# Kernel optimization log

Measured on AMD Instinct MI355X. Metric: run time of the kernel, lower is better.

The kernel has to match this reference:

```python
import jax, jax.numpy as jnp
import numpy as np

B, H, W, C = 16, 56, 56, 384
HEADS, WIN, SHIFT = 12, 7, 3
HD = C // HEADS
HIDDEN = 4 * C
NWH, NWW = H // WIN, W // WIN
NW = NWH * NWW
WA = WIN * WIN  # 49 tokens per window


def _rel_pos_index():
    coords = np.stack(np.meshgrid(np.arange(WIN), np.arange(WIN), indexing='ij')).reshape(2, -1)
    rel = coords[:, :, None] - coords[:, None, :]          # [2, WA, WA]
    rel = rel.transpose(1, 2, 0)
    rel[:, :, 0] += WIN - 1
    rel[:, :, 1] += WIN - 1
    rel[:, :, 0] *= 2 * WIN - 1
    return rel.sum(-1)                                      # [WA, WA]


def _attn_mask():
    img = np.zeros((H, W))
    cnt = 0
    for hs in (slice(0, -WIN), slice(-WIN, -SHIFT), slice(-SHIFT, None)):
        for ws in (slice(0, -WIN), slice(-WIN, -SHIFT), slice(-SHIFT, None)):
            img[hs, ws] = cnt
            cnt += 1
    mw = img.reshape(NWH, WIN, NWW, WIN).transpose(0, 2, 1, 3).reshape(NW, WA)
    diff = mw[:, None, :] - mw[:, :, None]
    return np.where(diff != 0, -100.0, 0.0).astype(np.float32)  # [NW, WA, WA]


REL_IDX = jnp.asarray(_rel_pos_index())
MASK = jnp.asarray(_attn_mask())


def _ln(x, g, b):
    m = x.mean(-1, keepdims=True)
    v = ((x - m) ** 2).mean(-1, keepdims=True)
    return (x - m) / jnp.sqrt(v + 1e-5) * g + b


def setup_inputs() -> dict:
    key = jax.random.key(0)
    ks = jax.random.split(key, 6)
    s = 0.02
    return {
        'x': jax.random.normal(ks[0], (B, H, W, C), jnp.float32),
        'norm1_g': jnp.ones((C,), jnp.float32),
        'norm1_b': jnp.zeros((C,), jnp.float32),
        'qkv_w': jax.random.normal(ks[1], (C, 3 * C), jnp.float32) * s,
        'qkv_b': jnp.zeros((3 * C,), jnp.float32),
        'rel_bias': jax.random.normal(ks[2], ((2 * WIN - 1) ** 2, HEADS), jnp.float32) * s,
        'proj_w': jax.random.normal(ks[3], (C, C), jnp.float32) * s,
        'proj_b': jnp.zeros((C,), jnp.float32),
        'norm2_g': jnp.ones((C,), jnp.float32),
        'norm2_b': jnp.zeros((C,), jnp.float32),
        'fc1_w': jax.random.normal(ks[4], (C, HIDDEN), jnp.float32) * s,
        'fc1_b': jnp.zeros((HIDDEN,), jnp.float32),
        'fc2_w': jax.random.normal(ks[5], (HIDDEN, C), jnp.float32) * s,
        'fc2_b': jnp.zeros((C,), jnp.float32),
    }


def reference(x, norm1_g, norm1_b, qkv_w, qkv_b, rel_bias, proj_w, proj_b,
              norm2_g, norm2_b, fc1_w, fc1_b, fc2_w, fc2_b):
    # ---- shifted-window attention branch ----
    xs = _ln(x, norm1_g, norm1_b)
    xs = jnp.roll(xs, (-SHIFT, -SHIFT), axis=(1, 2))
    # window partition: [B,H,W,C] -> [B*NW, WA, C]
    xw = xs.reshape(B, NWH, WIN, NWW, WIN, C).transpose(0, 1, 3, 2, 4, 5).reshape(B * NW, WA, C)
    qkv = (xw @ qkv_w + qkv_b).reshape(B * NW, WA, 3, HEADS, HD)
    q = qkv[:, :, 0].transpose(0, 2, 1, 3)  # [bw, heads, WA, HD]
    k = qkv[:, :, 1].transpose(0, 2, 1, 3)
    v = qkv[:, :, 2].transpose(0, 2, 1, 3)
    attn = jnp.einsum('bhqd,bhkd->bhqk', q, k) * (HD ** -0.5)
    bias = rel_bias[REL_IDX].transpose(2, 0, 1)  # [heads, WA, WA]
    attn = attn + bias[None]
    attn = attn.reshape(B, NW, HEADS, WA, WA) + MASK[None, :, None]
    attn = jax.nn.softmax(attn, axis=-1).reshape(B * NW, HEADS, WA, WA)
    out = jnp.einsum('bhqk,bhkd->bhqd', attn, v).transpose(0, 2, 1, 3).reshape(B * NW, WA, C)
    out = out @ proj_w + proj_b
    # window reverse + unshift
    out = out.reshape(B, NWH, NWW, WIN, WIN, C).transpose(0, 1, 3, 2, 4, 5).reshape(B, H, W, C)
    out = jnp.roll(out, (SHIFT, SHIFT), axis=(1, 2))
    x = x + out
    # ---- MLP branch ----
    xf = x.reshape(B, H * W, C)
    h = _ln(xf, norm2_g, norm2_b)
    h = jax.nn.gelu(h @ fc1_w + fc1_b, approximate=False)
    xf = xf + (h @ fc2_w + fc2_b)
    return xf.reshape(B, H, W, C)
```

## Files before the change

### kernel.cpp

```cpp
#include <hip/hip_runtime.h>
#include <hip/hip_bf16.h>
#include <math.h>

#define NBATCH 16
#define NW 64
#define WA 49
#define NTOK (NBATCH*NW*WA)
#define CCH 384
#define HIDDEN 1536

typedef __attribute__((ext_vector_type(8))) short short8;
typedef __attribute__((ext_vector_type(4))) float floatx4;

static __device__ __forceinline__ short f2bf(float f){
  unsigned u = __float_as_uint(f);
  unsigned r = (u + 0x7fff + ((u>>16)&1)) >> 16;
  return (short)r;
}
static __device__ __forceinline__ float bf2f(short s){
  return __uint_as_float(((unsigned)(unsigned short)s)<<16);
}

static __device__ __forceinline__ void gload16(const void* g, void* l){
  __builtin_amdgcn_global_load_lds(
      (const __attribute__((address_space(1))) void*)g,
      (__attribute__((address_space(3))) void*)l, 16, 0, 0);
}

static __device__ __forceinline__ short8 ds_read_b128s(unsigned addr){
  short8 r;
  asm volatile("ds_read_b128 %0, %1" : "=v"(r) : "v"(addr));
  return r;
}
static __device__ __forceinline__ long ds_read_b64s(unsigned addr){
  long r;
  asm volatile("ds_read_b64 %0, %1" : "=v"(r) : "v"(addr));
  return r;
}

template<int N> __device__ __forceinline__ void waitvm();
template<> __device__ __forceinline__ void waitvm<0>(){ asm volatile("s_waitcnt vmcnt(0)" ::: "memory"); }
template<> __device__ __forceinline__ void waitvm<5>(){ asm volatile("s_waitcnt vmcnt(5)" ::: "memory"); }

static __device__ __forceinline__ int tok2pix(int t){
  int b = t / (NW*WA);
  int rem = t % (NW*WA);
  int w = rem / WA, a = rem % WA;
  int hs = (w>>3)*7 + a/7;
  int ws = (w&7)*7 + a%7;
  int hp = hs + 3; if (hp >= 56) hp -= 56;
  int wp = ws + 3; if (wp >= 56) wp -= 56;
  return (b*56 + hp)*56 + wp;
}

__global__ void wtconv(const float* __restrict__ W, short* __restrict__ Wt, int K, int N){
  int i = blockIdx.x*256 + threadIdx.x;
  if (i >= K*N) return;
  int k = i / N, n = i % N;
  Wt[(size_t)n*K + k] = f2bf(W[i]);
}

__global__ void wtconv8(const float* __restrict__ W, unsigned char* __restrict__ Wt, int K, int N){
  int i = blockIdx.x*256 + threadIdx.x;
  if (i >= K*N) return;
  int k = i / N, n = i % N;
  unsigned pk = (unsigned)__builtin_amdgcn_cvt_pk_fp8_f32(W[i], W[i], 0, false);
  Wt[(size_t)n*K + k] = (unsigned char)(pk & 0xff);
}

__global__ void rbt(const float* __restrict__ rb, float* __restrict__ rbT){
  int i = blockIdx.x*256 + threadIdx.x;
  if (i >= 169*12) return;
  int t = i / 12, h = i % 12;
  rbT[h*169 + t] = rb[i];
}

template<int MAP>
__global__ __launch_bounds__(256) void ln_fp8(const float* __restrict__ x,
    const float* __restrict__ g, const float* __restrict__ bta, unsigned char* __restrict__ out){
  int wid = threadIdx.x>>6, lane = threadIdx.x&63;
  int t = blockIdx.x*4 + wid;
  const float* row = x + (size_t)(MAP ? tok2pix(t) : t)*CCH;
  float v[8]; float s=0.f, ss=0.f;
  if (lane < 48){
    float4 p0 = *(const float4*)&row[lane*8];
    float4 p1 = *(const float4*)&row[lane*8+4];
    v[0]=p0.x;v[1]=p0.y;v[2]=p0.z;v[3]=p0.w;
    v[4]=p1.x;v[5]=p1.y;v[6]=p1.z;v[7]=p1.w;
    #pragma unroll
    for (int i=0;i<8;i++){ s+=v[i]; ss+=v[i]*v[i]; }
  }
  #pragma unroll
  for (int off=32; off; off>>=1){ s += __shfl_xor(s,off); ss += __shfl_xor(ss,off); }
  float mean = s*(1.f/384.f);
  float var  = ss*(1.f/384.f) - mean*mean;
  float inv  = rsqrtf(var + 1e-5f);
  if (lane < 48){
    float4 g0 = *(const float4*)&g[lane*8],  g1 = *(const float4*)&g[lane*8+4];
    float4 b0 = *(const float4*)&bta[lane*8],b1 = *(const float4*)&bta[lane*8+4];
    float o[8];
    o[0]=(v[0]-mean)*inv*g0.x+b0.x; o[1]=(v[1]-mean)*inv*g0.y+b0.y;
    o[2]=(v[2]-mean)*inv*g0.z+b0.z; o[3]=(v[3]-mean)*inv*g0.w+b0.w;
    o[4]=(v[4]-mean)*inv*g1.x+b1.x; o[5]=(v[5]-mean)*inv*g1.y+b1.y;
    o[6]=(v[6]-mean)*inv*g1.z+b1.z; o[7]=(v[7]-mean)*inv*g1.w+b1.w;
    unsigned w0 = (unsigned)__builtin_amdgcn_cvt_pk_fp8_f32(o[0], o[1], 0, false);
    w0 = (unsigned)__builtin_amdgcn_cvt_pk_fp8_f32(o[2], o[3], (int)w0, true);
    unsigned w1 = (unsigned)__builtin_amdgcn_cvt_pk_fp8_f32(o[4], o[5], 0, false);
    w1 = (unsigned)__builtin_amdgcn_cvt_pk_fp8_f32(o[6], o[7], (int)w1, true);
    uint2 pk; pk.x = w0; pk.y = w1;
    *(uint2*)&out[(size_t)t*CCH + lane*8] = pk;
  }
}

template<int EPI, int KK>
__global__ __launch_bounds__(512) void gemm8(const short* __restrict__ A,
    const short* __restrict__ Bt, const float* __restrict__ bias,
    const float* __restrict__ res, void* __restrict__ outp,
    int N, int gx)
{
  __shared__ short As[2][256][64];
  __shared__ short Bs[2][64][64];
  const int tid = threadIdx.x, lane = tid & 63, wid = tid >> 6;
  const int fr = lane & 15, fg = lane >> 4;
  const int wm = wid >> 1, wn = wid & 1;

  const int nwg = gridDim.x;
  const int q = nwg >> 3, r = nwg & 7;
  const int xcd = blockIdx.x & 7, pos = blockIdx.x >> 3;
  const int wgid = (xcd < r ? xcd*(q+1) : r*(q+1) + (xcd-r)*q) + pos;
  const int m0 = (wgid / gx) * 256, n0 = (wgid % gx) * 64;

  floatx4 acc[4][2];
  #pragma unroll
  for (int m=0;m<4;m++)
    #pragma unroll
    for (int n=0;n<2;n++) acc[m][n] = (floatx4){0.f,0.f,0.f,0.f};

  const int srow = tid >> 3;
  const int scol = ((tid & 7) ^ (srow & 7)) * 8;
  const short* gA = A  + (size_t)(m0 + srow) * KK + scol;
  const short* gB = Bt + (size_t)(n0 + srow) * KK + scol;
  constexpr int a64 = 64 * KK;
  short* aB = &As[0][wid*8][0];
  short* bB = &Bs[0][wid*8][0];
  constexpr int nt = KK >> 6;

  const unsigned aLds = (unsigned)(uintptr_t)&As[0][0][0];
  const unsigned bLds = (unsigned)(uintptr_t)&Bs[0][0][0];
  const unsigned rowOffA = (unsigned)((wm*64 + fr)*128);
  const unsigned rowOffB = (unsigned)((wn*32 + fr)*128);
  const unsigned pc0 = (unsigned)(((fg  ) ^ (fr&7))*16);
  const unsigned pc1 = (unsigned)(((4+fg) ^ (fr&7))*16);

#define STAGE(tt, bb) do{                                             \
    const int k0_ = (tt) << 6;                                        \
    short* a_ = aB + (bb)*256*64;                                     \
    short* b_ = bB + (bb)*64*64;                                      \
    gload16(gA + k0_,          a_);                                   \
    gload16(gA + k0_ +   a64,  a_ +  64*64);                          \
    gload16(gA + k0_ + 2*a64,  a_ + 128*64);                          \
    gload16(gA + k0_ + 3*a64,  a_ + 192*64);                          \
    gload16(gB + k0_,          b_);                                   \
  }while(0)

  STAGE(0, 0);
  #pragma unroll
  for (int t = 0; t < nt; ++t){
    const int buf = t & 1;
    if (t + 1 < nt){
      STAGE(t+1, buf^1);
      waitvm<5>();
    } else {
      waitvm<0>();
    }
    __builtin_amdgcn_s_barrier();
    const unsigned aoff = aLds + (unsigned)buf*32768u + rowOffA;
    const unsigned boff = bLds + (unsigned)buf*8192u  + rowOffB;
    #pragma unroll
    for (int kk=0; kk<2; ++kk){
      const unsigned pc = kk ? pc1 : pc0;
      short8 af[4], bq[2];
      #pragma unroll
      for (int m=0;m<4;m++) af[m] = ds_read_b128s(aoff + (unsigned)(m*2048) + pc);
      #pragma unroll
      for (int n=0;n<2;n++) bq[n] = ds_read_b128s(boff + (unsigned)(n*2048) + pc);
      asm volatile("s_waitcnt lgkmcnt(0)" ::: "memory");
      __builtin_amdgcn_sched_barrier(0);
      __builtin_amdgcn_s_setprio(1);
      #pragma unroll
      for (int m=0;m<4;m++)
        #pragma unroll
        for (int n=0;n<2;n++)
          acc[m][n] = __builtin_amdgcn_mfma_f32_16x16x32_bf16(af[m], bq[n], acc[m][n], 0,0,0);
      __builtin_amdgcn_s_setprio(0);
    }
    __builtin_amdgcn_s_barrier();
  }
#undef STAGE

  __syncthreads();
  float* Cl = (float*)&As[0][0][0];
  #pragma unroll
  for (int n=0;n<2;n++){
    int col = wn*32 + n*16 + fr;
    float bv = bias[n0 + col];
    #pragma unroll
    for (int m=0;m<4;m++){
      #pragma unroll
      for (int i=0;i<4;i++){
        int row = wm*64 + m*16 + fg*4 + i;
        Cl[row*64 + col] = acc[m][n][i] + bv;
      }
    }
  }
  __syncthreads();
  const int rr = tid >> 4, slot = tid & 15;
  #pragma unroll
  for (int it=0; it<8; ++it){
    int row = it*32 + rr;
    float4 v = *(const float4*)&Cl[row*64 + slot*4];
    int p = tok2pix(m0+row);
    size_t idx = (size_t)p*CCH + n0 + slot*4;
    float4 rv = *(const float4*)&res[idx];
    v.x += rv.x; v.y += rv.y; v.z += rv.z; v.w += rv.w;
    *(float4*)&((float*)outp)[idx] = v;
  }
}

template<int EPI, int KK>
__global__ __launch_bounds__(512) void gemmF8(const unsigned char* __restrict__ A8,
    const unsigned char* __restrict__ B8, const float* __restrict__ bias,
    const float* __restrict__ res, void* __restrict__ outp,
    int N, int gx)
{
  __shared__ unsigned char As8[2][256][128];
  __shared__ unsigned char Bs8[2][64][128];
  const int tid = threadIdx.x, lane = tid & 63, wid = tid >> 6;
  const int fr = lane & 15, fg = lane >> 4;
  const int wm = wid >> 1, wn = wid & 1;

  const int nwg = gridDim.x;
  const int q = nwg >> 3, r = nwg & 7;
  const int xcd = blockIdx.x & 7, pos = blockIdx.x >> 3;
  const int wgid = (xcd < r ? xcd*(q+1) : r*(q+1) + (xcd-r)*q) + pos;
  const int m0 = (wgid / gx) * 256, n0 = (wgid % gx) * 64;

  floatx4 acc[4][2];
  #pragma unroll
  for (int m=0;m<4;m++)
    #pragma unroll
    for (int n=0;n<2;n++) acc[m][n] = (floatx4){0.f,0.f,0.f,0.f};

  const int srow = tid >> 3;
  const int scolb = ((tid & 7) ^ (srow & 7)) * 16;
  const unsigned char* gA = A8 + (size_t)(m0 + srow) * KK + scolb;
  const unsigned char* gB = B8 + (size_t)(n0 + srow) * KK + scolb;
  constexpr int a64 = 64 * KK;
  unsigned char* aB = &As8[0][wid*8][0];
  unsigned char* bB = &Bs8[0][wid*8][0];
  constexpr int nt = KK >> 7;

  const unsigned aLds = (unsigned)(uintptr_t)&As8[0][0][0];
  const unsigned bLds = (unsigned)(uintptr_t)&Bs8[0][0][0];
  const unsigned rowOffA = (unsigned)((wm*64 + fr)*128);
  const unsigned rowOffB = (unsigned)((wn*32 + fr)*128);
  unsigned pcc[4];
  #pragma unroll
  for (int kk=0;kk<4;kk++)
    pcc[kk] = (unsigned)((((kk*2 + (fg>>1)) ^ (fr&7))*16) + (fg&1)*8);

#define STAGE8(tt, bb) do{                                            \
    const int k0_ = (tt) << 7;                                        \
    unsigned char* a_ = aB + (bb)*256*128;                            \
    unsigned char* b_ = bB + (bb)*64*128;                             \
    gload16(gA + k0_,          a_);                                   \
    gload16(gA + k0_ +   a64,  a_ +  8192);                           \
    gload16(gA + k0_ + 2*a64,  a_ + 16384);                           \
    gload16(gA + k0_ + 3*a64,  a_ + 24576);                           \
    gload16(gB + k0_,          b_);                                   \
  }while(0)

  STAGE8(0, 0);
  #pragma unroll
  for (int t = 0; t < nt; ++t){
    const int buf = t & 1;
    if (t + 1 < nt){
      STAGE8(t+1, buf^1);
      waitvm<5>();
    } else {
      waitvm<0>();
    }
    __builtin_amdgcn_s_barrier();
    const unsigned aoff = aLds + (unsigned)buf*32768u + rowOffA;
    const unsigned boff = bLds + (unsigned)buf*8192u  + rowOffB;
    #pragma unroll
    for (int kk=0; kk<4; ++kk){
      const unsigned pc = pcc[kk];
      long af[4], bq[2];
      #pragma unroll
      for (int m=0;m<4;m++) af[m] = ds_read_b64s(aoff + (unsigned)(m*2048) + pc);
      #pragma unroll
      for (int n=0;n<2;n++) bq[n] = ds_read_b64s(boff + (unsigned)(n*2048) + pc);
      asm volatile("s_waitcnt lgkmcnt(0)" ::: "memory");
      __builtin_amdgcn_sched_barrier(0);
      __builtin_amdgcn_s_setprio(1);
      #pragma unroll
      for (int m=0;m<4;m++)
        #pragma unroll
        for (int n=0;n<2;n++)
          acc[m][n] = __builtin_amdgcn_mfma_f32_16x16x32_fp8_fp8(af[m], bq[n], acc[m][n], 0,0,0);
      __builtin_amdgcn_s_setprio(0);
    }
    __builtin_amdgcn_s_barrier();
  }
#undef STAGE8

  __syncthreads();
  if (EPI==0){
    short* Cl = (short*)&As8[0][0][0];
    #pragma unroll
    for (int n=0;n<2;n++){
      int col = wn*32 + n*16 + fr;
      float bv = bias[n0 + col];
      #pragma unroll
      for (int m=0;m<4;m++){
        #pragma unroll
        for (int i=0;i<4;i++){
          int row = wm*64 + m*16 + fg*4 + i;
          Cl[row*64 + col] = f2bf(acc[m][n][i] + bv);
        }
      }
    }
    __syncthreads();
    const int rr = tid >> 3, slot = tid & 7;
    #pragma unroll
    for (int it=0; it<4; ++it){
      int row = it*64 + rr;
      short8 v = *(const short8*)&Cl[row*64 + slot*8];
      *(short8*)&((short*)outp)[(size_t)(m0+row)*N + n0 + slot*8] = v;
    }
  } else if (EPI==2){
    unsigned char* Cl = (unsigned char*)&As8[0][0][0];
    #pragma unroll
    for (int n=0;n<2;n++){
      int col = wn*32 + n*16 + fr;
      float bv = bias[n0 + col];
      #pragma unroll
      for (int m=0;m<4;m++){
        #pragma unroll
        for (int i=0;i<4;i++){
          int row = wm*64 + m*16 + fg*4 + i;
          float v = acc[m][n][i] + bv;
          float e2 = __expf(-1.702f*v);
          float gg = v * __builtin_amdgcn_rcpf(1.f + e2);
          unsigned pk = (unsigned)__builtin_amdgcn_cvt_pk_fp8_f32(gg, gg, 0, false);
          Cl[row*64 + col] = (unsigned char)(pk & 0xff);
        }
      }
    }
    __syncthreads();
    const int rr = tid >> 2, slot = tid & 3;
    #pragma unroll
    for (int it=0; it<2; ++it){
      int row = it*128 + rr;
      short8 v = *(const short8*)&Cl[row*64 + slot*16];
      *(short8*)&((unsigned char*)outp)[(size_t)(m0+row)*N + n0 + slot*16] = v;
    }
  } else {
    float* Cl = (float*)&As8[0][0][0];
    #pragma unroll
    for (int n=0;n<2;n++){
      int col = wn*32 + n*16 + fr;
      float bv = bias[n0 + col];
      #pragma unroll
      for (int m=0;m<4;m++){
        #pragma unroll
        for (int i=0;i<4;i++){
          int row = wm*64 + m*16 + fg*4 + i;
          Cl[row*64 + col] = acc[m][n][i] + bv;
        }
      }
    }
    __syncthreads();
    const int rr = tid >> 4, slot = tid & 15;
    #pragma unroll
    for (int it=0; it<8; ++it){
      int row = it*32 + rr;
      float4 v = *(const float4*)&Cl[row*64 + slot*4];
      size_t idx = (size_t)(m0+row)*CCH + n0 + slot*4;
      float4 rv = *(const float4*)&res[idx];
      v.x += rv.x; v.y += rv.y; v.z += rv.z; v.w += rv.w;
      *(float4*)&((float*)outp)[idx] = v;
    }
  }
}

__global__ __launch_bounds__(256) void attn_mfma(const short* __restrict__ qkv,
    const float* __restrict__ rbT, short* __restrict__ attnout)
{
  __shared__ short Pl[4][64][68];
  __shared__ short Vt[4][32][68];
  __shared__ float lb[4][169];
  __shared__ int grp[64];
  const int wi = blockIdx.x;
  const int wid = threadIdx.x>>6, lane = threadIdx.x&63;
  const int fr = lane&15, fg = lane>>4;
  const int w = wi & 63, wh = w>>3, ww = w&7;
  if (threadIdx.x < 64){
    int t = threadIdx.x;
    int gv = 0;
    if (t < 49){
      int ai = t/7, aj = t%7;
      int hs = wh*7+ai, ws = ww*7+aj;
      int gh = hs<49?0:(hs<53?1:2);
      int gw = ws<49?0:(ws<53?1:2);
      gv = gh*3+gw;
    } else gv = -1;
    grp[t] = gv;
  }
  for (int t = lane; t < 32*15; t += 64){
    int d = t/15, j = 49 + t - d*15;
    Vt[wid][d][j] = 0;
  }
  __syncthreads();
  const size_t tbase = (size_t)wi*49;
  const float SCALE = 0.17677669529663687f;

  for (int hi=0; hi<3; ++hi){
    const int h = hi*4 + wid;
    for (int t = lane; t < 169; t += 64) lb[wid][t] = rbT[h*169 + t];
    for (int t = lane; t < 196; t += 64){
      int j = t>>2, d0 = (t&3)*8;
      short8 vv = *(const short8*)&qkv[(tbase+j)*1152 + 768 + h*32 + d0];
      #pragma unroll
      for (int s=0;s<8;s++) Vt[wid][d0+s][j] = vv[s];
    }
    short8 zf = {};
    short8 aq[4], bk[4];
    #pragma unroll
    for (int m=0;m<4;m++){
      int r = m*16+fr;
      aq[m] = (r<49) ? *(const short8*)&qkv[(tbase+r)*1152       + h*32 + fg*8] : zf;
      bk[m] = (r<49) ? *(const short8*)&qkv[(tbase+r)*1152 + 384 + h*32 + fg*8] : zf;
    }

    floatx4 sc[4][4];
    #pragma unroll
    for (int m=0;m<4;m++)
      #pragma unroll
      for (int n=0;n<4;n++)
        sc[m][n] = __builtin_amdgcn_mfma_f32_16x16x32_bf16(aq[m], bk[n], (floatx4){0.f,0.f,0.f,0.f}, 0,0,0);

    int ciC[4], cjC[4], gC[4], cvC[4];
    #pragma unroll
    for (int n=0;n<4;n++){
      int c = n*16+fr;
      ciC[n] = c/7; cjC[n] = c - ciC[n]*7;
      gC[n] = grp[c]; cvC[n] = (c<49);
    }
    #pragma unroll
    for (int m=0;m<4;m++){
      #pragma unroll
      for (int i=0;i<4;i++){
        int r = m*16 + fg*4 + i;
        int rv = (r<49);
        int ri = r/7, rj = r - ri*7;
        int gr = grp[r];
        float mxv = -3e30f;
        #pragma unroll
        for (int n=0;n<4;n++){
          float s;
          if (rv && cvC[n]){
            int dr = ri - ciC[n] + 6, dc = rj - cjC[n] + 6;
            s = sc[m][n][i]*SCALE + lb[wid][dr*13+dc];
            if (gr != gC[n]) s -= 100.f;
          } else s = -3e30f;
          sc[m][n][i] = s;
          mxv = fmaxf(mxv, s);
        }
        #pragma unroll
        for (int off=1;off<16;off<<=1) mxv = fmaxf(mxv, __shfl_xor(mxv, off));
        float sum = 0.f;
        #pragma unroll
        for (int n=0;n<4;n++){
          float e = __expf(sc[m][n][i]-mxv);
          sc[m][n][i] = e; sum += e;
        }
        #pragma unroll
        for (int off=1;off<16;off<<=1) sum += __shfl_xor(sum, off);
        float inv = 1.f/sum;
        #pragma unroll
        for (int n=0;n<4;n++)
          Pl[wid][r][n*16+fr] = f2bf(sc[m][n][i]*inv);
      }
    }

    short8 pa[4][2], vb[2][2];
    #pragma unroll
    for (int m=0;m<4;m++)
      #pragma unroll
      for (int ks=0;ks<2;ks++)
        pa[m][ks] = *(const short8*)&Pl[wid][m*16+fr][ks*32+fg*8];
    #pragma unroll
    for (int n2=0;n2<2;n2++)
      #pragma unroll
      for (int ks=0;ks<2;ks++)
        vb[n2][ks] = *(const short8*)&Vt[wid][n2*16+fr][ks*32+fg*8];
    floatx4 oc[4][2];
    #pragma unroll
    for (int m=0;m<4;m++)
      #pragma unroll
      for (int n2=0;n2<2;n2++){
        oc[m][n2] = (floatx4){0.f,0.f,0.f,0.f};
        #pragma unroll
        for (int ks=0;ks<2;ks++)
          oc[m][n2] = __builtin_amdgcn_mfma_f32_16x16x32_bf16(pa[m][ks], vb[n2][ks], oc[m][n2], 0,0,0);
      }
    #pragma unroll
    for (int m=0;m<4;m++){
      #pragma unroll
      for (int i=0;i<4;i++){
        int r = m*16 + fg*4 + i;
        if (r < 49){
          #pragma unroll
          for (int n2=0;n2<2;n2++)
            attnout[(tbase+r)*384 + h*32 + n2*16 + fr] = f2bf(oc[m][n2][i]);
        }
      }
    }
  }
}

extern "C" void kernel_launch(void* const* d_in, const int* in_sizes, int n_in,
                              void* d_out, int out_size, void* d_ws, size_t ws_size,
                              hipStream_t stream)
{
  const float* x      = (const float*)d_in[0];
  const float* n1g    = (const float*)d_in[1];
  const float* n1b    = (const float*)d_in[2];
  const float* qkv_w  = (const float*)d_in[3];
  const float* qkv_b  = (const float*)d_in[4];
  const float* relb   = (const float*)d_in[5];
  const float* proj_w = (const float*)d_in[6];
  const float* proj_b = (const float*)d_in[7];
  const float* n2g    = (const float*)d_in[8];
  const float* n2b    = (const float*)d_in[9];
  const float* fc1_w  = (const float*)d_in[10];
  const float* fc1_b  = (const float*)d_in[11];
  const float* fc2_w  = (const float*)d_in[12];
  const float* fc2_b  = (const float*)d_in[13];

  char* ws = (char*)d_ws;
  const size_t SZ_XW  = (size_t)NTOK*CCH*2;
  const size_t SZ_QKV = (size_t)NTOK*1152*2;
  const size_t SZ_ATT = SZ_XW;
  const size_t SZ_Y   = (size_t)NTOK*CCH*4;

  unsigned char* xw8 = (unsigned char*)(ws);
  short* qkvb  = (short*)(ws + SZ_XW);
  short* att   = (short*)(ws + SZ_XW + SZ_QKV);
  float* y     = (float*)(ws + SZ_XW + SZ_QKV + SZ_ATT);
  char*  wbuf  = ws + SZ_XW + SZ_QKV + SZ_ATT + SZ_Y;
  unsigned char* qkvW8 = (unsigned char*)wbuf;
  short* projWt        = (short*)(qkvW8 + (size_t)1152*384);
  unsigned char* fc1W8 = (unsigned char*)(projWt + (size_t)384*384);
  unsigned char* fc2W8 = fc1W8 + (size_t)1536*384;
  float* rbT           = (float*)(fc2W8 + (size_t)384*1536);
  unsigned char* hbuf8 = (unsigned char*)qkvb;
  unsigned char* hin8  = xw8;

  wtconv8<<<dim3((384*1152+255)/256), dim3(256), 0, stream>>>(qkv_w, qkvW8, 384, 1152);
  wtconv<<<dim3((384*384 +255)/256), dim3(256), 0, stream>>>(proj_w, projWt, 384, 384);
  wtconv8<<<dim3((384*1536+255)/256), dim3(256), 0, stream>>>(fc1_w, fc1W8, 384, 1536);
  wtconv8<<<dim3((1536*384+255)/256), dim3(256), 0, stream>>>(fc2_w, fc2W8, 1536, 384);
  rbt<<<dim3((169*12+255)/256), dim3(256), 0, stream>>>(relb, rbT);

  ln_fp8<1><<<dim3(NTOK/4), dim3(256), 0, stream>>>(x, n1g, n1b, xw8);
  gemmF8<0,384><<<dim3(18*196), dim3(512), 0, stream>>>(xw8, qkvW8, qkv_b, nullptr, qkvb, 1152, 18);
  attn_mfma<<<dim3(NBATCH*NW), dim3(256), 0, stream>>>(qkvb, rbT, att);
  gemm8<1,384><<<dim3(6*196),  dim3(512), 0, stream>>>(att, projWt, proj_b, x, y, 384, 6);
  ln_fp8<0><<<dim3(NTOK/4), dim3(256), 0, stream>>>(y, n2g, n2b, hin8);
  gemmF8<2,384><<<dim3(24*196), dim3(512), 0, stream>>>(hin8, fc1W8, fc1_b, nullptr, hbuf8, 1536, 24);
  gemmF8<3,1536><<<dim3(6*196), dim3(512), 0, stream>>>(hbuf8, fc2W8, fc2_b, y, (float*)d_out, 384, 6);
}
```

Measured before the change: 352.5 us.

## Move attention path (qkv, attention, proj) from bf16 to fp8

The QKV GEMM now writes fp8 output, with the softmax scale folded into Q in its epilogue. The attention kernel reads fp8 Q/K/V and runs fp8 MFMAs for both QK^T and PV, storing P and the attention output as fp8. The proj GEMM reuses the fp8 GEMM with a new epilogue that does the window-reverse scatter and residual add. This halves memory traffic for the intermediates and uses faster fp8 matrix ops, at the cost of more quantization error in the attention probabilities and values.

```diff
diff --git a/kernel.cpp b/kernel.cpp
--- a/kernel.cpp
+++ b/kernel.cpp
@@ -17,9 +17,6 @@
   unsigned r = (u + 0x7fff + ((u>>16)&1)) >> 16;
   return (short)r;
 }
-static __device__ __forceinline__ float bf2f(short s){
-  return __uint_as_float(((unsigned)(unsigned short)s)<<16);
-}
 
 static __device__ __forceinline__ void gload16(const void* g, void* l){
   __builtin_amdgcn_global_load_lds(
@@ -27,11 +24,6 @@
       (__attribute__((address_space(3))) void*)l, 16, 0, 0);
 }
 
-static __device__ __forceinline__ short8 ds_read_b128s(unsigned addr){
-  short8 r;
-  asm volatile("ds_read_b128 %0, %1" : "=v"(r) : "v"(addr));
-  return r;
-}
 static __device__ __forceinline__ long ds_read_b64s(unsigned addr){
   long r;
   asm volatile("ds_read_b64 %0, %1" : "=v"(r) : "v"(addr));
@@ -51,13 +43,6 @@
   int hp = hs + 3; if (hp >= 56) hp -= 56;
   int wp = ws + 3; if (wp >= 56) wp -= 56;
   return (b*56 + hp)*56 + wp;
-}
-
-__global__ void wtconv(const float* __restrict__ W, short* __restrict__ Wt, int K, int N){
-  int i = blockIdx.x*256 + threadIdx.x;
-  if (i >= K*N) return;
-  int k = i / N, n = i % N;
-  Wt[(size_t)n*K + k] = f2bf(W[i]);
 }
 
 __global__ void wtconv8(const float* __restrict__ W, unsigned char* __restrict__ Wt, int K, int N){
@@ -113,121 +98,6 @@
 }
 
 template<int EPI, int KK>
-__global__ __launch_bounds__(512) void gemm8(const short* __restrict__ A,
-    const short* __restrict__ Bt, const float* __restrict__ bias,
-    const float* __restrict__ res, void* __restrict__ outp,
-    int N, int gx)
-{
-  __shared__ short As[2][256][64];
-  __shared__ short Bs[2][64][64];
-  const int tid = threadIdx.x, lane = tid & 63, wid = tid >> 6;
-  const int fr = lane & 15, fg = lane >> 4;
-  const int wm = wid >> 1, wn = wid & 1;
-
-  const int nwg = gridDim.x;
-  const int q = nwg >> 3, r = nwg & 7;
-  const int xcd = blockIdx.x & 7, pos = blockIdx.x >> 3;
-  const int wgid = (xcd < r ? xcd*(q+1) : r*(q+1) + (xcd-r)*q) + pos;
-  const int m0 = (wgid / gx) * 256, n0 = (wgid % gx) * 64;
-
-  floatx4 acc[4][2];
-  #pragma unroll
-  for (int m=0;m<4;m++)
-    #pragma unroll
-    for (int n=0;n<2;n++) acc[m][n] = (floatx4){0.f,0.f,0.f,0.f};
-
-  const int srow = tid >> 3;
-  const int scol = ((tid & 7) ^ (srow & 7)) * 8;
-  const short* gA = A  + (size_t)(m0 + srow) * KK + scol;
-  const short* gB = Bt + (size_t)(n0 + srow) * KK + scol;
-  constexpr int a64 = 64 * KK;
-  short* aB = &As[0][wid*8][0];
-  short* bB = &Bs[0][wid*8][0];
-  constexpr int nt = KK >> 6;
-
-  const unsigned aLds = (unsigned)(uintptr_t)&As[0][0][0];
-  const unsigned bLds = (unsigned)(uintptr_t)&Bs[0][0][0];
-  const unsigned rowOffA = (unsigned)((wm*64 + fr)*128);
-  const unsigned rowOffB = (unsigned)((wn*32 + fr)*128);
-  const unsigned pc0 = (unsigned)(((fg  ) ^ (fr&7))*16);
-  const unsigned pc1 = (unsigned)(((4+fg) ^ (fr&7))*16);
-
-#define STAGE(tt, bb) do{                                             \
-    const int k0_ = (tt) << 6;                                        \
-    short* a_ = aB + (bb)*256*64;                                     \
-    short* b_ = bB + (bb)*64*64;                                      \
-    gload16(gA + k0_,          a_);                                   \
-    gload16(gA + k0_ +   a64,  a_ +  64*64);                          \
-    gload16(gA + k0_ + 2*a64,  a_ + 128*64);                          \
-    gload16(gA + k0_ + 3*a64,  a_ + 192*64);                          \
-    gload16(gB + k0_,          b_);                                   \
-  }while(0)
-
-  STAGE(0, 0);
-  #pragma unroll
-  for (int t = 0; t < nt; ++t){
-    const int buf = t & 1;
-    if (t + 1 < nt){
-      STAGE(t+1, buf^1);
-      waitvm<5>();
-    } else {
-      waitvm<0>();
-    }
-    __builtin_amdgcn_s_barrier();
-    const unsigned aoff = aLds + (unsigned)buf*32768u + rowOffA;
-    const unsigned boff = bLds + (unsigned)buf*8192u  + rowOffB;
-    #pragma unroll
-    for (int kk=0; kk<2; ++kk){
-      const unsigned pc = kk ? pc1 : pc0;
-      short8 af[4], bq[2];
-      #pragma unroll
-      for (int m=0;m<4;m++) af[m] = ds_read_b128s(aoff + (unsigned)(m*2048) + pc);
-      #pragma unroll
-      for (int n=0;n<2;n++) bq[n] = ds_read_b128s(boff + (unsigned)(n*2048) + pc);
-      asm volatile("s_waitcnt lgkmcnt(0)" ::: "memory");
-      __builtin_amdgcn_sched_barrier(0);
-      __builtin_amdgcn_s_setprio(1);
-      #pragma unroll
-      for (int m=0;m<4;m++)
-        #pragma unroll
-        for (int n=0;n<2;n++)
-          acc[m][n] = __builtin_amdgcn_mfma_f32_16x16x32_bf16(af[m], bq[n], acc[m][n], 0,0,0);
-      __builtin_amdgcn_s_setprio(0);
-    }
-    __builtin_amdgcn_s_barrier();
-  }
-#undef STAGE
-
-  __syncthreads();
-  float* Cl = (float*)&As[0][0][0];
-  #pragma unroll
-  for (int n=0;n<2;n++){
-    int col = wn*32 + n*16 + fr;
-    float bv = bias[n0 + col];
-    #pragma unroll
-    for (int m=0;m<4;m++){
-      #pragma unroll
-      for (int i=0;i<4;i++){
-        int row = wm*64 + m*16 + fg*4 + i;
-        Cl[row*64 + col] = acc[m][n][i] + bv;
-      }
-    }
-  }
-  __syncthreads();
-  const int rr = tid >> 4, slot = tid & 15;
-  #pragma unroll
-  for (int it=0; it<8; ++it){
-    int row = it*32 + rr;
-    float4 v = *(const float4*)&Cl[row*64 + slot*4];
-    int p = tok2pix(m0+row);
-    size_t idx = (size_t)p*CCH + n0 + slot*4;
-    float4 rv = *(const float4*)&res[idx];
-    v.x += rv.x; v.y += rv.y; v.z += rv.z; v.w += rv.w;
-    *(float4*)&((float*)outp)[idx] = v;
-  }
-}
-
-template<int EPI, int KK>
 __global__ __launch_bounds__(512) void gemmF8(const unsigned char* __restrict__ A8,
     const unsigned char* __restrict__ B8, const float* __restrict__ bias,
     const float* __restrict__ res, void* __restrict__ outp,
@@ -316,8 +186,9 @@
 #undef STAGE8
 
   __syncthreads();
-  if (EPI==0){
-    short* Cl = (short*)&As8[0][0][0];
+  if (EPI==2 || EPI==4){
+    unsigned char* Cl = (unsigned char*)&As8[0][0][0];
+    const float qscale = (EPI==4 && n0 < 384) ? 0.17677669529663687f : 1.f;
     #pragma unroll
     for (int n=0;n<2;n++){
       int col = wn*32 + n*16 + fr;
@@ -327,33 +198,14 @@
         #pragma unroll
         for (int i=0;i<4;i++){
           int row = wm*64 + m*16 + fg*4 + i;
-          Cl[row*64 + col] = f2bf(acc[m][n][i] + bv);
-        }
-      }
-    }
-    __syncthreads();
-    const int rr = tid >> 3, slot = tid & 7;
-    #pragma unroll
-    for (int it=0; it<4; ++it){
-      int row = it*64 + rr;
-      short8 v = *(const short8*)&Cl[row*64 + slot*8];
-      *(short8*)&((short*)outp)[(size_t)(m0+row)*N + n0 + slot*8] = v;
-    }
-  } else if (EPI==2){
-    unsigned char* Cl = (unsigned char*)&As8[0][0][0];
-    #pragma unroll
-    for (int n=0;n<2;n++){
-      int col = wn*32 + n*16 + fr;
-      float bv = bias[n0 + col];
-      #pragma unroll
-      for (int m=0;m<4;m++){
-        #pragma unroll
-        for (int i=0;i<4;i++){
-          int row = wm*64 + m*16 + fg*4 + i;
           float v = acc[m][n][i] + bv;
-          float e2 = __expf(-1.702f*v);
-          float gg = v * __builtin_amdgcn_rcpf(1.f + e2);
-          unsigned pk = (unsigned)__builtin_amdgcn_cvt_pk_fp8_f32(gg, gg, 0, false);
+          if (EPI==2){
+            float e2 = __expf(-1.702f*v);
+            v = v * __builtin_amdgcn_rcpf(1.f + e2);
+          } else {
+            v *= qscale;
+          }
+          unsigned pk = (unsigned)__builtin_amdgcn_cvt_pk_fp8_f32(v, v, 0, false);
           Cl[row*64 + col] = (unsigned char)(pk & 0xff);
         }
       }
@@ -387,7 +239,13 @@
     for (int it=0; it<8; ++it){
       int row = it*32 + rr;
       float4 v = *(const float4*)&Cl[row*64 + slot*4];
-      size_t idx = (size_t)(m0+row)*CCH + n0 + slot*4;
+      size_t idx;
+      if (EPI==5){
+        int p = tok2pix(m0+row);
+        idx = (size_t)p*CCH + n0 + slot*4;
+      } else {
+        idx = (size_t)(m0+row)*CCH + n0 + slot*4;
+      }
       float4 rv = *(const float4*)&res[idx];
       v.x += rv.x; v.y += rv.y; v.z += rv.z; v.w += rv.w;
       *(float4*)&((float*)outp)[idx] = v;
@@ -395,11 +253,11 @@
   }
 }
 
-__global__ __launch_bounds__(256) void attn_mfma(const short* __restrict__ qkv,
-    const float* __restrict__ rbT, short* __restrict__ attnout)
+__global__ __launch_bounds__(256) void attn_mfma8(const unsigned char* __restrict__ qkv8,
+    const float* __restrict__ rbT, unsigned char* __restrict__ att8)
 {
-  __shared__ short Pl[4][64][68];
-  __shared__ short Vt[4][32][68];
+  __shared__ unsigned char Pl[4][64][72];
+  __shared__ unsigned char Vt[4][32][72];
   __shared__ float lb[4][169];
   __shared__ int grp[64];
   const int wi = blockIdx.x;
@@ -418,30 +276,26 @@
     } else gv = -1;
     grp[t] = gv;
   }
-  for (int t = lane; t < 32*15; t += 64){
-    int d = t/15, j = 49 + t - d*15;
-    Vt[wid][d][j] = 0;
-  }
+  for (int t = lane; t < 288; t += 64)
+    ((long*)&Vt[wid][0][0])[t] = 0;
   __syncthreads();
   const size_t tbase = (size_t)wi*49;
-  const float SCALE = 0.17677669529663687f;
 
   for (int hi=0; hi<3; ++hi){
     const int h = hi*4 + wid;
     for (int t = lane; t < 169; t += 64) lb[wid][t] = rbT[h*169 + t];
     for (int t = lane; t < 196; t += 64){
       int j = t>>2, d0 = (t&3)*8;
-      short8 vv = *(const short8*)&qkv[(tbase+j)*1152 + 768 + h*32 + d0];
-      #pragma unroll
-      for (int s=0;s<8;s++) Vt[wid][d0+s][j] = vv[s];
-    }
-    short8 zf = {};
-    short8 aq[4], bk[4];
+      unsigned long vv = *(const unsigned long*)&qkv8[(tbase+j)*1152 + 768 + h*32 + d0];
+      #pragma unroll
+      for (int s=0;s<8;s++) Vt[wid][d0+s][j] = (unsigned char)(vv >> (8*s));
+    }
+    long aq[4], bk[4];
     #pragma unroll
     for (int m=0;m<4;m++){
       int r = m*16+fr;
-      aq[m] = (r<49) ? *(const short8*)&qkv[(tbase+r)*1152       + h*32 + fg*8] : zf;
-      bk[m] = (r<49) ? *(const short8*)&qkv[(tbase+r)*1152 + 384 + h*32 + fg*8] : zf;
+      aq[m] = (r<49) ? *(const long*)&qkv8[(tbase+r)*1152       + h*32 + fg*8] : 0L;
+      bk[m] = (r<49) ? *(const long*)&qkv8[(tbase+r)*1152 + 384 + h*32 + fg*8] : 0L;
     }
 
     floatx4 sc[4][4];
@@ -449,7 +303,7 @@
     for (int m=0;m<4;m++)
       #pragma unroll
       for (int n=0;n<4;n++)
-        sc[m][n] = __builtin_amdgcn_mfma_f32_16x16x32_bf16(aq[m], bk[n], (floatx4){0.f,0.f,0.f,0.f}, 0,0,0);
+        sc[m][n] = __builtin_amdgcn_mfma_f32_16x16x32_fp8_fp8(aq[m], bk[n], (floatx4){0.f,0.f,0.f,0.f}, 0,0,0);
 
     int ciC[4], cjC[4], gC[4], cvC[4];
     #pragma unroll
@@ -472,7 +326,7 @@
           float s;
           if (rv && cvC[n]){
             int dr = ri - ciC[n] + 6, dc = rj - cjC[n] + 6;
-            s = sc[m][n][i]*SCALE + lb[wid][dr*13+dc];
+            s = sc[m][n][i] + lb[wid][dr*13+dc];
             if (gr != gC[n]) s -= 100.f;
           } else s = -3e30f;
           sc[m][n][i] = s;
@@ -490,22 +344,25 @@
         for (int off=1;off<16;off<<=1) sum += __shfl_xor(sum, off);
         float inv = 1.f/sum;
         #pragma unroll
-        for (int n=0;n<4;n++)
-          Pl[wid][r][n*16+fr] = f2bf(sc[m][n][i]*inv);
-      }
-    }
-
-    short8 pa[4][2], vb[2][2];
+        for (int n=0;n<4;n++){
+          float p = sc[m][n][i]*inv;
+          unsigned pk = (unsigned)__builtin_amdgcn_cvt_pk_fp8_f32(p, p, 0, false);
+          Pl[wid][r][n*16+fr] = (unsigned char)(pk & 0xff);
+        }
+      }
+    }
+
+    long pa[4][2], vb[2][2];
     #pragma unroll
     for (int m=0;m<4;m++)
       #pragma unroll
       for (int ks=0;ks<2;ks++)
-        pa[m][ks] = *(const short8*)&Pl[wid][m*16+fr][ks*32+fg*8];
+        pa[m][ks] = *(const long*)&Pl[wid][m*16+fr][ks*32+fg*8];
     #pragma unroll
     for (int n2=0;n2<2;n2++)
       #pragma unroll
       for (int ks=0;ks<2;ks++)
-        vb[n2][ks] = *(const short8*)&Vt[wid][n2*16+fr][ks*32+fg*8];
+        vb[n2][ks] = *(const long*)&Vt[wid][n2*16+fr][ks*32+fg*8];
     floatx4 oc[4][2];
     #pragma unroll
     for (int m=0;m<4;m++)
@@ -514,7 +371,7 @@
         oc[m][n2] = (floatx4){0.f,0.f,0.f,0.f};
         #pragma unroll
         for (int ks=0;ks<2;ks++)
-          oc[m][n2] = __builtin_amdgcn_mfma_f32_16x16x32_bf16(pa[m][ks], vb[n2][ks], oc[m][n2], 0,0,0);
+          oc[m][n2] = __builtin_amdgcn_mfma_f32_16x16x32_fp8_fp8(pa[m][ks], vb[n2][ks], oc[m][n2], 0,0,0);
       }
     #pragma unroll
     for (int m=0;m<4;m++){
@@ -523,8 +380,11 @@
         int r = m*16 + fg*4 + i;
         if (r < 49){
           #pragma unroll
-          for (int n2=0;n2<2;n2++)
-            attnout[(tbase+r)*384 + h*32 + n2*16 + fr] = f2bf(oc[m][n2][i]);
+          for (int n2=0;n2<2;n2++){
+            float v = oc[m][n2][i];
+            unsigned pk = (unsigned)__builtin_amdgcn_cvt_pk_fp8_f32(v, v, 0, false);
+            att8[(tbase+r)*384 + h*32 + n2*16 + fr] = (unsigned char)(pk & 0xff);
+          }
         }
       }
     }
@@ -556,29 +416,29 @@
   const size_t SZ_ATT = SZ_XW;
   const size_t SZ_Y   = (size_t)NTOK*CCH*4;
 
-  unsigned char* xw8 = (unsigned char*)(ws);
-  short* qkvb  = (short*)(ws + SZ_XW);
-  short* att   = (short*)(ws + SZ_XW + SZ_QKV);
+  unsigned char* xw8  = (unsigned char*)(ws);
+  unsigned char* qkv8 = (unsigned char*)(ws + SZ_XW);
+  unsigned char* att8 = (unsigned char*)(ws + SZ_XW + SZ_QKV);
   float* y     = (float*)(ws + SZ_XW + SZ_QKV + SZ_ATT);
   char*  wbuf  = ws + SZ_XW + SZ_QKV + SZ_ATT + SZ_Y;
   unsigned char* qkvW8 = (unsigned char*)wbuf;
-  short* projWt        = (short*)(qkvW8 + (size_t)1152*384);
-  unsigned char* fc1W8 = (unsigned char*)(projWt + (size_t)384*384);
+  unsigned char* projW8= qkvW8 + (size_t)1152*384;
+  unsigned char* fc1W8 = projW8 + (size_t)384*384;
   unsigned char* fc2W8 = fc1W8 + (size_t)1536*384;
   float* rbT           = (float*)(fc2W8 + (size_t)384*1536);
-  unsigned char* hbuf8 = (unsigned char*)qkvb;
+  unsigned char* hbuf8 = qkv8;
   unsigned char* hin8  = xw8;
 
   wtconv8<<<dim3((384*1152+255)/256), dim3(256), 0, stream>>>(qkv_w, qkvW8, 384, 1152);
-  wtconv<<<dim3((384*384 +255)/256), dim3(256), 0, stream>>>(proj_w, projWt, 384, 384);
+  wtconv8<<<dim3((384*384 +255)/256), dim3(256), 0, stream>>>(proj_w, projW8, 384, 384);
   wtconv8<<<dim3((384*1536+255)/256), dim3(256), 0, stream>>>(fc1_w, fc1W8, 384, 1536);
   wtconv8<<<dim3((1536*384+255)/256), dim3(256), 0, stream>>>(fc2_w, fc2W8, 1536, 384);
   rbt<<<dim3((169*12+255)/256), dim3(256), 0, stream>>>(relb, rbT);
 
   ln_fp8<1><<<dim3(NTOK/4), dim3(256), 0, stream>>>(x, n1g, n1b, xw8);
-  gemmF8<0,384><<<dim3(18*196), dim3(512), 0, stream>>>(xw8, qkvW8, qkv_b, nullptr, qkvb, 1152, 18);
-  attn_mfma<<<dim3(NBATCH*NW), dim3(256), 0, stream>>>(qkvb, rbT, att);
-  gemm8<1,384><<<dim3(6*196),  dim3(512), 0, stream>>>(att, projWt, proj_b, x, y, 384, 6);
+  gemmF8<4,384><<<dim3(18*196), dim3(512), 0, stream>>>(xw8, qkvW8, qkv_b, nullptr, qkv8, 1152, 18);
+  attn_mfma8<<<dim3(NBATCH*NW), dim3(256), 0, stream>>>(qkv8, rbT, att8);
+  gemmF8<5,384><<<dim3(6*196),  dim3(512), 0, stream>>>(att8, projW8, proj_b, x, y, 384, 6);
   ln_fp8<0><<<dim3(NTOK/4), dim3(256), 0, stream>>>(y, n2g, n2b, hin8);
   gemmF8<2,384><<<dim3(24*196), dim3(512), 0, stream>>>(hin8, fc1W8, fc1_b, nullptr, hbuf8, 1536, 24);
   gemmF8<3,1536><<<dim3(6*196), dim3(512), 0, stream>>>(hbuf8, fc2W8, fc2_b, y, (float*)d_out, 384, 6);
```

Measured after the change: 333.2 us. 1.06x faster.
